# Kernel tuning notes

Measured on AMD Instinct MI355X. Metric: run time of the kernel, lower is better.

The kernel has to match this reference:

```python
import jax, jax.numpy as jnp
import numpy as np

B, T, N, FIN, FOUT, EDGE_DIM = 8, 16, 256, 32, 32, 16


def setup_inputs() -> dict:
    key = jax.random.key(0)
    ks = jax.random.split(key, 8)
    def xavier(k, shape):
        fan_in, fan_out = shape[0], shape[1]
        limit = float(np.sqrt(6.0 / (fan_in + fan_out)))
        return jax.random.uniform(k, shape, jnp.float32, -limit, limit)
    return {
        "x": jax.random.normal(ks[0], (B, T, N, FIN), jnp.float32),
        "adj": jax.random.uniform(ks[1], (N, N), jnp.float32),
        # edge_net: Linear(1, edge_dim) -> GELU -> Linear(edge_dim, Fin*Fout)
        "w1": xavier(ks[2], (1, EDGE_DIM)),
        "b1": jnp.zeros((EDGE_DIM,), jnp.float32),
        "w2": xavier(ks[3], (EDGE_DIM, FIN * FOUT)),
        "b2": jnp.zeros((FIN * FOUT,), jnp.float32),
        # node_lin: Linear(Fin, Fout)
        "node_w": xavier(ks[4], (FIN, FOUT)),
        "node_b": jnp.zeros((FOUT,), jnp.float32),
    }


def reference(x, adj, w1, b1, w2, b2, node_w, node_b):
    # edge-conditioned weights: (N, N, Fin, Fout)
    h = jax.nn.gelu(adj[:, :, None] * w1[0] + b1, approximate=False)  # (N,N,E)
    edge_w = (h @ w2 + b2).reshape(N, N, FIN, FOUT)
    # msg[b,t,i,j,:] = sum_f x[b,t,j,f] * edge_w[i,j,f,:]; agg = sum_j msg
    agg = jnp.einsum("btjf,ijfo->btio", x, edge_w)  # (B,T,N,Fout)
    y = jax.nn.gelu(x @ node_w + node_b + agg, approximate=False)
    return y
```

## Files before the change

### kernel.cpp

```cpp
#include <hip/hip_runtime.h>
#include <math.h>

#define NB    256
#define EDIM  16
#define FINN  32
#define FOUTN 32
#define BT    128


typedef __attribute__((ext_vector_type(8))) short short8;
typedef __attribute__((ext_vector_type(4))) float floatx4;

#define MFMA16(a,b,c) __builtin_amdgcn_mfma_f32_16x16x32_bf16((a),(b),(c),0,0,0)

__device__ __forceinline__ float gelu_f(float v) {
    return 0.5f * v * (1.0f + erff(v * 0.70710678118654752f));
}
__device__ __forceinline__ ushort f2bf(float x) {
    union { float f; unsigned u; } v; v.f = x;
    unsigned r = (v.u + 0x7FFFu + ((v.u >> 16) & 1u)) >> 16;
    return (ushort)r;
}
__device__ __forceinline__ uint2 pack4(floatx4 d) {
    uint2 p;
    p.x = (unsigned)f2bf(d[0]) | ((unsigned)f2bf(d[1]) << 16);
    p.y = (unsigned)f2bf(d[2]) | ((unsigned)f2bf(d[3]) << 16);
    return p;
}

typedef __attribute__((address_space(1))) void gvoid_t;
typedef __attribute__((address_space(3))) void lvoid_t;
__device__ __forceinline__ void gload_lds16(const void* g, void* l) {
    __builtin_amdgcn_global_load_lds((gvoid_t*)g, (lvoid_t*)l, 16, 0, 0);
}

__global__ __launch_bounds__(256) void prep_kernel(
        const float* __restrict__ x,   const float* __restrict__ adj,
        const float* __restrict__ w1,  const float* __restrict__ b1,
        const float* __restrict__ w2,  const float* __restrict__ b2,
        const float* __restrict__ node_w, const float* __restrict__ node_b,
        ushort* __restrict__ Hf, ushort* __restrict__ y2f,
        float* __restrict__ bias2g, ushort* __restrict__ nwf) {
    int bid = blockIdx.x;
    int tid = threadIdx.x;
    __shared__ float adjs[16][264];
    __shared__ float w1s[16], b1s[16];
    __shared__ float Sp[8][32];
    __shared__ float Svs[32];

    if (bid < 1024) {
        int bt = bid >> 3, ep = bid & 7;
        int wv = tid >> 6, lane = tid & 63, m = lane & 15, quad = lane >> 4;
        short8 xf[4];
        #pragma unroll
        for (int t = 0; t < 4; ++t) {
            int jt = wv * 4 + t;
            const float* xs = x + ((size_t)bt * NB + jt * 16 + m) * FINN + quad * 8;
            float4 lo = *(const float4*)xs;
            float4 hi = *(const float4*)(xs + 4);
            ushort tmp[8];
            tmp[0]=f2bf(lo.x); tmp[1]=f2bf(lo.y); tmp[2]=f2bf(lo.z); tmp[3]=f2bf(lo.w);
            tmp[4]=f2bf(hi.x); tmp[5]=f2bf(hi.y); tmp[6]=f2bf(hi.z); tmp[7]=f2bf(hi.w);
            xf[t] = *(short8*)tmp;
        }
        #pragma unroll
        for (int ee = 0; ee < 2; ++ee) {
            int e = ep * 2 + ee;
            short8 wf[2];
            #pragma unroll
            for (int ot = 0; ot < 2; ++ot) {
                ushort tmp[8];
                #pragma unroll
                for (int d = 0; d < 8; ++d)
                    tmp[d] = f2bf(w2[(size_t)e * 1024 + (quad * 8 + d) * 32 + ot * 16 + m]);
                wf[ot] = *(short8*)tmp;
            }
            #pragma unroll
            for (int t = 0; t < 4; ++t) {
                int jt = wv * 4 + t;
                floatx4 z = {0.f, 0.f, 0.f, 0.f};
                floatx4 d0 = MFMA16(xf[t], wf[0], z);
                floatx4 d1 = MFMA16(xf[t], wf[1], z);
                int ks = e * 8 + (jt >> 1);
                int qp = (jt & 1) * 2 + (quad >> 1);
                int dp = (quad & 1) * 4;
                size_t base = ((size_t)bt * 128 + ks) * 1024;
                *(uint2*)(y2f + base +       (qp * 16 + m) * 8 + dp) = pack4(d0);
                *(uint2*)(y2f + base + 512 + (qp * 16 + m) * 8 + dp) = pack4(d1);
            }
        }
        if (ep == 0) {
            int f = tid & 31, grp = tid >> 5;
            float s = 0.f;
            for (int j = grp; j < NB; j += 8)
                s += x[((size_t)bt * NB + j) * FINN + f];
            Sp[grp][f] = s;
            __syncthreads();
            if (tid < 32) {
                float s2 = 0.f;
                #pragma unroll
                for (int g = 0; g < 8; ++g) s2 += Sp[g][tid];
                Svs[tid] = s2;
            }
            __syncthreads();
            if (tid < 32) {
                float bb = node_b[tid];
                #pragma unroll
                for (int f2 = 0; f2 < FINN; ++f2)
                    bb += Svs[f2] * b2[f2 * FOUTN + tid];
                bias2g[bt * 32 + tid] = bb;
            }
        }
        return;
    }
    if (bid < 1152) {
        int hb = bid - 1024;
        int it = hb & 15;
        int kq = hb >> 4;
        if (tid < 16) { w1s[tid] = w1[tid]; b1s[tid] = b1[tid]; }
        #pragma unroll
        for (int q = 0; q < 4; ++q) {
            int u = q * 256 + tid;
            int row = u >> 6, c4 = u & 63;
            *(float4*)&adjs[row][c4 * 4] =
                ((const float4*)(adj + ((size_t)it * 16 + row) * 256))[c4];
        }
        __syncthreads();
        #pragma unroll
        for (int q = 0; q < 4; ++q) {
            int u = q * 256 + tid;
            int ks = kq * 16 + (u >> 6);
            int lane = u & 63;
            int m = lane & 15, quad = lane >> 4;
            int e = ks >> 3;
            int j0 = (ks & 7) * 32 + quad * 8;
            float w = w1s[e], b = b1s[e];
            ushort tmp[8];
            #pragma unroll
            for (int d = 0; d < 8; ++d)
                tmp[d] = f2bf(gelu_f(adjs[m][j0 + d] * w + b));
            *(int4*)(Hf + (((size_t)it * 128 + ks) * 64 + lane) * 8) = *(int4*)tmp;
        }
        return;
    }
    if (tid < 128) {
        int ot = tid >> 6, lane = tid & 63, m = lane & 15, q = lane >> 4;
        ushort tmp[8];
        #pragma unroll
        for (int d = 0; d < 8; ++d)
            tmp[d] = f2bf(node_w[(q * 8 + d) * 32 + ot * 16 + m]);
        *(int4*)(nwf + tid * 8) = *(int4*)tmp;
    }
}

__global__ __launch_bounds__(512, 2) void fused_kernel(
        const float* __restrict__ x,      const ushort* __restrict__ Hf,
        const ushort* __restrict__ y2f,   const float* __restrict__ bias2g,
        const ushort* __restrict__ nwf,   float* __restrict__ out) {
    __shared__ ushort Bsl[2][16][2][64][8];

    int bt   = blockIdx.x;
    int iq2  = blockIdx.y;
    int tid  = threadIdx.x;
    int wv   = tid >> 6;
    int lane = tid & 63;
    int m    = lane & 15;
    int quad = lane >> 4;
    int it   = iq2 * 8 + wv;
    int i0g  = it * 16;

    const ushort* Hlane = Hf + (size_t)it * 65536 + lane * 8;
    const ushort* y2bt  = y2f + (size_t)bt * 131072;

    floatx4 acc[2] = {};

    #define STAGE(buf, c)                                                     \
    {                                                                         \
        const ushort* s_ = y2bt + (size_t)(c) * 16384;                        \
        ushort* d_ = &Bsl[buf][0][0][0][0];                                   \
        _Pragma("unroll")                                                     \
        for (int s = 0; s < 4; ++s)                                           \
            gload_lds16(s_ + s * 4096 + tid * 8, d_ + s * 4096 + tid * 8);    \
    }
    #define GEMMC(buf, c)                                                     \
    {                                                                         \
        _Pragma("unroll")                                                     \
        for (int kk = 0; kk < 16; ++kk) {                                     \
            short8 a  = *(const short8*)(Hlane + ((c) * 16 + kk) * 512);      \
            short8 b0 = *(const short8*)&Bsl[buf][kk][0][lane][0];            \
            short8 b1 = *(const short8*)&Bsl[buf][kk][1][lane][0];            \
            acc[0] = MFMA16(a, b0, acc[0]);                                   \
            acc[1] = MFMA16(a, b1, acc[1]);                                   \
        }                                                                     \
    }

    STAGE(0, 0);
    __syncthreads();
    #pragma unroll
    for (int c = 0; c < 8; ++c) {
        if (c < 7) STAGE((c + 1) & 1, c + 1);
        GEMMC(c & 1, c);
        __syncthreads();
    }

    short8 xa;
    {
        const float* xs = x + ((size_t)bt * NB + i0g + m) * FINN + quad * 8;
        float4 lo = *(const float4*)xs;
        float4 hi = *(const float4*)(xs + 4);
        ushort tmp[8];
        tmp[0]=f2bf(lo.x); tmp[1]=f2bf(lo.y); tmp[2]=f2bf(lo.z); tmp[3]=f2bf(lo.w);
        tmp[4]=f2bf(hi.x); tmp[5]=f2bf(hi.y); tmp[6]=f2bf(hi.z); tmp[7]=f2bf(hi.w);
        xa = *(short8*)tmp;
    }
    #pragma unroll
    for (int tn = 0; tn < 2; ++tn) {
        short8 nb = *(const short8*)(nwf + (tn * 64 + lane) * 8);
        acc[tn] = MFMA16(xa, nb, acc[tn]);
    }
    #pragma unroll
    for (int tn = 0; tn < 2; ++tn) {
        int o = tn * 16 + m;
        float bz = bias2g[bt * 32 + o];
        #pragma unroll
        for (int r = 0; r < 4; ++r) {
            int row = i0g + quad * 4 + r;
            out[((size_t)bt * NB + row) * FOUTN + o] = gelu_f(acc[tn][r] + bz);
        }
    }
    #undef STAGE
    #undef GEMMC
}

extern "C" void kernel_launch(void* const* d_in, const int* in_sizes, int n_in,
                              void* d_out, int out_size, void* d_ws, size_t ws_size,
                              hipStream_t stream) {
    const float* x      = (const float*)d_in[0];
    const float* adj    = (const float*)d_in[1];
    const float* w1     = (const float*)d_in[2];
    const float* b1     = (const float*)d_in[3];
    const float* w2     = (const float*)d_in[4];
    const float* b2     = (const float*)d_in[5];
    const float* node_w = (const float*)d_in[6];
    const float* node_b = (const float*)d_in[7];
    float* out = (float*)d_out;

    ushort* Hf     = (ushort*)d_ws;
    ushort* y2f    = Hf + (size_t)(1 << 20);
    float*  bias2g = (float*)(y2f + (size_t)(1 << 24));
    ushort* nwf    = (ushort*)(bias2g + 128 * 32);

    hipLaunchKernelGGL(prep_kernel, dim3(1153), dim3(256), 0, stream,
                       x, adj, w1, b1, w2, b2, node_w, node_b,
                       Hf, y2f, bias2g, nwf);
    hipLaunchKernelGGL(fused_kernel, dim3(BT, 2), dim3(512), 0, stream,
                       x, Hf, y2f, bias2g, nwf, out);
}
```

Baseline: 111.5 us.

## Compute x·W2 products on the fly inside the main GEMM, add split-K and an epilogue kernel

```diff
diff --git a/kernel.cpp b/kernel.cpp
--- a/kernel.cpp
+++ b/kernel.cpp
@@ -2,7 +2,6 @@
 #include <math.h>
 
 #define NB    256
-#define EDIM  16
 #define FINN  32
 #define FOUTN 32
 #define BT    128
@@ -39,109 +38,94 @@
         const float* __restrict__ w1,  const float* __restrict__ b1,
         const float* __restrict__ w2,  const float* __restrict__ b2,
         const float* __restrict__ node_w, const float* __restrict__ node_b,
-        ushort* __restrict__ Hf, ushort* __restrict__ y2f,
-        float* __restrict__ bias2g, ushort* __restrict__ nwf) {
+        ushort* __restrict__ Hf, ushort* __restrict__ w2f,
+        ushort* __restrict__ xaf, ushort* __restrict__ nwf,
+        float* __restrict__ bias2g) {
     int bid = blockIdx.x;
     int tid = threadIdx.x;
-    __shared__ float adjs[16][264];
-    __shared__ float w1s[16], b1s[16];
-    __shared__ float Sp[8][32];
-    __shared__ float Svs[32];
-
-    if (bid < 1024) {
-        int bt = bid >> 3, ep = bid & 7;
+
+    if (bid < 128) {
+        __shared__ float adjs[16][264];
+        __shared__ float w1s[16], b1s[16];
+        int it = bid & 15;
+        int kq8 = bid >> 4;
+        if (tid < 16) { w1s[tid] = w1[tid]; b1s[tid] = b1[tid]; }
+        #pragma unroll
+        for (int q = 0; q < 4; ++q) {
+            int u = q * 256 + tid;
+            int row = u >> 6, c4 = u & 63;
+            *(float4*)&adjs[row][c4 * 4] =
+                ((const float4*)(adj + ((size_t)it * 16 + row) * 256))[c4];
+        }
+        __syncthreads();
+        #pragma unroll
+        for (int q = 0; q < 4; ++q) {
+            int u = q * 256 + tid;
+            int ks = kq8 * 16 + (u >> 6);
+            int lane = u & 63;
+            int m = lane & 15, quad = lane >> 4;
+            int e = ks >> 3;
+            int j0 = (ks & 7) * 32 + quad * 8;
+            float w = w1s[e], b = b1s[e];
+            ushort tmp[8];
+            #pragma unroll
+            for (int d = 0; d < 8; ++d)
+                tmp[d] = f2bf(gelu_f(adjs[m][j0 + d] * w + b));
+            *(int4*)(Hf + (((size_t)it * 128 + ks) * 64 + lane) * 8) = *(int4*)tmp;
+        }
+        return;
+    }
+    if (bid < 160) {
         int wv = tid >> 6, lane = tid & 63, m = lane & 15, quad = lane >> 4;
-        short8 xf[4];
-        #pragma unroll
-        for (int t = 0; t < 4; ++t) {
-            int jt = wv * 4 + t;
+        int bt = (bid - 128) * 4 + wv;
+        #pragma unroll
+        for (int jt = 0; jt < 16; ++jt) {
             const float* xs = x + ((size_t)bt * NB + jt * 16 + m) * FINN + quad * 8;
             float4 lo = *(const float4*)xs;
             float4 hi = *(const float4*)(xs + 4);
             ushort tmp[8];
             tmp[0]=f2bf(lo.x); tmp[1]=f2bf(lo.y); tmp[2]=f2bf(lo.z); tmp[3]=f2bf(lo.w);
             tmp[4]=f2bf(hi.x); tmp[5]=f2bf(hi.y); tmp[6]=f2bf(hi.z); tmp[7]=f2bf(hi.w);
-            xf[t] = *(short8*)tmp;
-        }
-        #pragma unroll
-        for (int ee = 0; ee < 2; ++ee) {
-            int e = ep * 2 + ee;
-            short8 wf[2];
-            #pragma unroll
-            for (int ot = 0; ot < 2; ++ot) {
-                ushort tmp[8];
-                #pragma unroll
-                for (int d = 0; d < 8; ++d)
-                    tmp[d] = f2bf(w2[(size_t)e * 1024 + (quad * 8 + d) * 32 + ot * 16 + m]);
-                wf[ot] = *(short8*)tmp;
-            }
-            #pragma unroll
-            for (int t = 0; t < 4; ++t) {
-                int jt = wv * 4 + t;
-                floatx4 z = {0.f, 0.f, 0.f, 0.f};
-                floatx4 d0 = MFMA16(xf[t], wf[0], z);
-                floatx4 d1 = MFMA16(xf[t], wf[1], z);
-                int ks = e * 8 + (jt >> 1);
-                int qp = (jt & 1) * 2 + (quad >> 1);
-                int dp = (quad & 1) * 4;
-                size_t base = ((size_t)bt * 128 + ks) * 1024;
-                *(uint2*)(y2f + base +       (qp * 16 + m) * 8 + dp) = pack4(d0);
-                *(uint2*)(y2f + base + 512 + (qp * 16 + m) * 8 + dp) = pack4(d1);
-            }
-        }
-        if (ep == 0) {
-            int f = tid & 31, grp = tid >> 5;
-            float s = 0.f;
-            for (int j = grp; j < NB; j += 8)
-                s += x[((size_t)bt * NB + j) * FINN + f];
-            Sp[grp][f] = s;
-            __syncthreads();
-            if (tid < 32) {
-                float s2 = 0.f;
-                #pragma unroll
-                for (int g = 0; g < 8; ++g) s2 += Sp[g][tid];
-                Svs[tid] = s2;
-            }
-            __syncthreads();
-            if (tid < 32) {
-                float bb = node_b[tid];
-                #pragma unroll
-                for (int f2 = 0; f2 < FINN; ++f2)
-                    bb += Svs[f2] * b2[f2 * FOUTN + tid];
-                bias2g[bt * 32 + tid] = bb;
-            }
+            *(int4*)(xaf + (((size_t)bt * 16 + jt) * 64 + lane) * 8) = *(int4*)tmp;
         }
         return;
     }
-    if (bid < 1152) {
-        int hb = bid - 1024;
-        int it = hb & 15;
-        int kq = hb >> 4;
-        if (tid < 16) { w1s[tid] = w1[tid]; b1s[tid] = b1[tid]; }
-        #pragma unroll
-        for (int q = 0; q < 4; ++q) {
-            int u = q * 256 + tid;
-            int row = u >> 6, c4 = u & 63;
-            *(float4*)&adjs[row][c4 * 4] =
-                ((const float4*)(adj + ((size_t)it * 16 + row) * 256))[c4];
-        }
-        __syncthreads();
-        #pragma unroll
-        for (int q = 0; q < 4; ++q) {
-            int u = q * 256 + tid;
-            int ks = kq * 16 + (u >> 6);
-            int lane = u & 63;
-            int m = lane & 15, quad = lane >> 4;
-            int e = ks >> 3;
-            int j0 = (ks & 7) * 32 + quad * 8;
-            float w = w1s[e], b = b1s[e];
-            ushort tmp[8];
-            #pragma unroll
-            for (int d = 0; d < 8; ++d)
-                tmp[d] = f2bf(gelu_f(adjs[m][j0 + d] * w + b));
-            *(int4*)(Hf + (((size_t)it * 128 + ks) * 64 + lane) * 8) = *(int4*)tmp;
+    if (bid < 288) {
+        __shared__ float Sp[8][32];
+        __shared__ float Svs[32];
+        int bt = bid - 160;
+        int f = tid & 31, grp = tid >> 5;
+        float s = 0.f;
+        for (int j = grp; j < NB; j += 8)
+            s += x[((size_t)bt * NB + j) * FINN + f];
+        Sp[grp][f] = s;
+        __syncthreads();
+        if (tid < 32) {
+            float s2 = 0.f;
+            #pragma unroll
+            for (int g = 0; g < 8; ++g) s2 += Sp[g][tid];
+            Svs[tid] = s2;
+        }
+        __syncthreads();
+        if (tid < 32) {
+            float bb = node_b[tid];
+            #pragma unroll
+            for (int f2 = 0; f2 < FINN; ++f2)
+                bb += Svs[f2] * b2[f2 * FOUTN + tid];
+            bias2g[bt * 32 + tid] = bb;
         }
         return;
+    }
+    for (int s = 0; s < 2048; s += 256) {
+        int slot = s + tid;
+        int e = slot >> 7, r = slot & 127;
+        int ot = r >> 6, lane = r & 63;
+        int m = lane & 15, quad = lane >> 4;
+        const float* src = w2 + (size_t)e * 1024 + (quad * 8) * 32 + ot * 16 + m;
+        ushort tmp[8];
+        #pragma unroll
+        for (int i = 0; i < 8; ++i) tmp[i] = f2bf(src[i * 32]);
+        *(int4*)(w2f + (size_t)slot * 8) = *(int4*)tmp;
     }
     if (tid < 128) {
         int ot = tid >> 6, lane = tid & 63, m = lane & 15, q = lane >> 4;
@@ -153,83 +137,135 @@
     }
 }
 
-__global__ __launch_bounds__(512, 2) void fused_kernel(
-        const float* __restrict__ x,      const ushort* __restrict__ Hf,
-        const ushort* __restrict__ y2f,   const float* __restrict__ bias2g,
-        const ushort* __restrict__ nwf,   float* __restrict__ out) {
-    __shared__ ushort Bsl[2][16][2][64][8];
-
-    int bt   = blockIdx.x;
-    int iq2  = blockIdx.y;
+__global__ __launch_bounds__(512, 1) void main_kernel(
+        const ushort* __restrict__ Hf,  const ushort* __restrict__ w2f,
+        const ushort* __restrict__ xaf, float* __restrict__ Cp) {
+    __shared__ ushort Asl[2][2][16][512];
+    __shared__ ushort Bsl[2][2][4][512];
+
+    int btq  = blockIdx.x;
+    int oh   = blockIdx.y;
+    int kq   = blockIdx.z;
     int tid  = threadIdx.x;
     int wv   = tid >> 6;
     int lane = tid & 63;
     int m    = lane & 15;
     int quad = lane >> 4;
-    int it   = iq2 * 8 + wv;
-    int i0g  = it * 16;
-
-    const ushort* Hlane = Hf + (size_t)it * 65536 + lane * 8;
-    const ushort* y2bt  = y2f + (size_t)bt * 131072;
-
-    floatx4 acc[2] = {};
-
-    #define STAGE(buf, c)                                                     \
-    {                                                                         \
-        const ushort* s_ = y2bt + (size_t)(c) * 16384;                        \
-        ushort* d_ = &Bsl[buf][0][0][0][0];                                   \
-        _Pragma("unroll")                                                     \
-        for (int s = 0; s < 4; ++s)                                           \
-            gload_lds16(s_ + s * 4096 + tid * 8, d_ + s * 4096 + tid * 8);    \
-    }
-    #define GEMMC(buf, c)                                                     \
+
+    int pbt = wv & 3;
+    int pjh = wv >> 2;
+    int btg = btq * 4 + pbt;
+
+    short8 xfr[8];
+    #pragma unroll
+    for (int p = 0; p < 8; ++p)
+        xfr[p] = *(const short8*)(xaf + (((size_t)btg * 16 + p * 2 + pjh) * 64 + lane) * 8);
+
+    floatx4 acc[2][4] = {};
+
+    #define STAGE_A(buf, c)                                                   \
     {                                                                         \
         _Pragma("unroll")                                                     \
-        for (int kk = 0; kk < 16; ++kk) {                                     \
-            short8 a  = *(const short8*)(Hlane + ((c) * 16 + kk) * 512);      \
-            short8 b0 = *(const short8*)&Bsl[buf][kk][0][lane][0];            \
-            short8 b1 = *(const short8*)&Bsl[buf][kk][1][lane][0];            \
-            acc[0] = MFMA16(a, b0, acc[0]);                                   \
-            acc[1] = MFMA16(a, b1, acc[1]);                                   \
+        for (int s = 0; s < 4; ++s) {                                         \
+            int fid = s * 8 + wv;                    \
+            int itA = fid & 15, ksL = fid >> 4;                               \
+            int ksg = kq * 32 + (c) * 2 + ksL;                                \
+            gload_lds16(Hf + (((size_t)itA * 128 + ksg) * 64 + lane) * 8,     \
+                        &Asl[buf][ksL][itA][lane * 8]);                       \
         }                                                                     \
     }
-
-    STAGE(0, 0);
+    #define PRODUCE(buf, c)                                                   \
+    {                                                                         \
+        _Pragma("unroll")                                                     \
+        for (int s = 0; s < 2; ++s) {                                         \
+            int ksg = kq * 32 + (c) * 2 + s;                                  \
+            int e = ksg >> 3, p = ksg & 7;                                    \
+            short8 wf = *(const short8*)(w2f + (size_t)e * 1024 + oh * 512 + lane * 8); \
+            floatx4 z = {0.f, 0.f, 0.f, 0.f};                                 \
+            floatx4 d = MFMA16(xfr[p], wf, z);                                \
+            int qc = pjh * 2 + (quad >> 1), dp = (quad & 1) * 4;              \
+            *(uint2*)&Bsl[buf][s][pbt][(qc * 16 + m) * 8 + dp] = pack4(d);    \
+        }                                                                     \
+    }
+    #define GEMMC(buf)                                                        \
+    {                                                                         \
+        _Pragma("unroll")                                                     \
+        for (int kk = 0; kk < 2; ++kk) {                                      \
+            short8 a0 = *(const short8*)&Asl[buf][kk][wv * 2 + 0][lane * 8];  \
+            short8 a1 = *(const short8*)&Asl[buf][kk][wv * 2 + 1][lane * 8];  \
+            _Pragma("unroll")                                                 \
+            for (int bb = 0; bb < 4; ++bb) {                                  \
+                short8 b = *(const short8*)&Bsl[buf][kk][bb][lane * 8];       \
+                acc[0][bb] = MFMA16(a0, b, acc[0][bb]);                       \
+                acc[1][bb] = MFMA16(a1, b, acc[1][bb]);                       \
+            }                                                                 \
+        }                                                                     \
+    }
+
+    STAGE_A(0, 0);
+    PRODUCE(0, 0);
     __syncthreads();
     #pragma unroll
-    for (int c = 0; c < 8; ++c) {
-        if (c < 7) STAGE((c + 1) & 1, c + 1);
-        GEMMC(c & 1, c);
-        __syncthreads();
-    }
-
-    short8 xa;
-    {
-        const float* xs = x + ((size_t)bt * NB + i0g + m) * FINN + quad * 8;
-        float4 lo = *(const float4*)xs;
-        float4 hi = *(const float4*)(xs + 4);
-        ushort tmp[8];
-        tmp[0]=f2bf(lo.x); tmp[1]=f2bf(lo.y); tmp[2]=f2bf(lo.z); tmp[3]=f2bf(lo.w);
-        tmp[4]=f2bf(hi.x); tmp[5]=f2bf(hi.y); tmp[6]=f2bf(hi.z); tmp[7]=f2bf(hi.w);
-        xa = *(short8*)tmp;
-    }
-    #pragma unroll
-    for (int tn = 0; tn < 2; ++tn) {
-        short8 nb = *(const short8*)(nwf + (tn * 64 + lane) * 8);
-        acc[tn] = MFMA16(xa, nb, acc[tn]);
-    }
-    #pragma unroll
-    for (int tn = 0; tn < 2; ++tn) {
-        int o = tn * 16 + m;
-        float bz = bias2g[bt * 32 + o];
-        #pragma unroll
-        for (int r = 0; r < 4; ++r) {
-            int row = i0g + quad * 4 + r;
-            out[((size_t)bt * NB + row) * FOUTN + o] = gelu_f(acc[tn][r] + bz);
-        }
-    }
-    #undef STAGE
+    for (int c = 0; c < 16; ++c) {
+        if (c < 15) {
+            STAGE_A((c + 1) & 1, c + 1);
+            PRODUCE((c + 1) & 1, c + 1);
+        }
+        GEMMC(c & 1);
+        __syncthreads();
+    }
+
+    #pragma unroll
+    for (int t = 0; t < 2; ++t) {
+        #pragma unroll
+        for (int bb = 0; bb < 4; ++bb) {
+            #pragma unroll
+            for (int r = 0; r < 4; ++r) {
+                int i = (wv * 2 + t) * 16 + quad * 4 + r;
+                Cp[(((size_t)kq * BT + btq * 4 + bb) * NB + i) * FOUTN + oh * 16 + m]
+                    = acc[t][bb][r];
+            }
+        }
+    }
+    #undef STAGE_A
+    #undef PRODUCE
     #undef GEMMC
+}
+
+__global__ __launch_bounds__(256) void epi_kernel(
+        const ushort* __restrict__ xaf, const ushort* __restrict__ nwf,
+        const float* __restrict__ bias2g, const float* __restrict__ Cp,
+        float* __restrict__ out) {
+    int bt   = blockIdx.x;
+    int tid  = threadIdx.x;
+    int wv   = tid >> 6;
+    int lane = tid & 63;
+    int m    = lane & 15;
+    int quad = lane >> 4;
+
+    short8 nb0 = *(const short8*)(nwf + (size_t)lane * 8);
+    short8 nb1 = *(const short8*)(nwf + ((size_t)64 + lane) * 8);
+
+    #pragma unroll
+    for (int t = 0; t < 4; ++t) {
+        int it = wv * 4 + t;
+        short8 xa = *(const short8*)(xaf + (((size_t)bt * 16 + it) * 64 + lane) * 8);
+        #pragma unroll
+        for (int tn = 0; tn < 2; ++tn) {
+            floatx4 z = {0.f, 0.f, 0.f, 0.f};
+            floatx4 ea = MFMA16(xa, tn ? nb1 : nb0, z);
+            float bz = bias2g[bt * 32 + tn * 16 + m];
+            #pragma unroll
+            for (int r = 0; r < 4; ++r) {
+                int i = it * 16 + quad * 4 + r;
+                float s = ea[r] + bz;
+                #pragma unroll
+                for (int kqi = 0; kqi < 4; ++kqi)
+                    s += Cp[(((size_t)kqi * BT + bt) * NB + i) * FOUTN + tn * 16 + m];
+                out[((size_t)bt * NB + i) * FOUTN + tn * 16 + m] = gelu_f(s);
+            }
+        }
+    }
 }
 
 extern "C" void kernel_launch(void* const* d_in, const int* in_sizes, int n_in,
@@ -246,13 +282,17 @@
     float* out = (float*)d_out;
 
     ushort* Hf     = (ushort*)d_ws;
-    ushort* y2f    = Hf + (size_t)(1 << 20);
-    float*  bias2g = (float*)(y2f + (size_t)(1 << 24));
-    ushort* nwf    = (ushort*)(bias2g + 128 * 32);
-
-    hipLaunchKernelGGL(prep_kernel, dim3(1153), dim3(256), 0, stream,
+    ushort* w2f    = Hf + (size_t)16 * 128 * 512;
+    ushort* xaf    = w2f + 16384;
+    ushort* nwf    = xaf + (size_t)128 * 16 * 512;
+    float*  bias2g = (float*)(nwf + 1024);
+    float*  Cp     = bias2g + 128 * 32;
+
+    hipLaunchKernelGGL(prep_kernel, dim3(289), dim3(256), 0, stream,
                        x, adj, w1, b1, w2, b2, node_w, node_b,
-                       Hf, y2f, bias2g, nwf);
-    hipLaunchKernelGGL(fused_kernel, dim3(BT, 2), dim3(512), 0, stream,
-                       x, Hf, y2f, bias2g, nwf, out);
-}
+                       Hf, w2f, xaf, nwf, bias2g);
+    hipLaunchKernelGGL(main_kernel, dim3(32, 2, 4), dim3(512), 0, stream,
+                       Hf, w2f, xaf, Cp);
+    hipLaunchKernelGGL(epi_kernel, dim3(BT), dim3(256), 0, stream,
+                       xaf, nwf, bias2g, Cp, out);
+}
```

After: 113.9 us. 2.2% more time.
